# Optimization experiments

Measured on AMD Instinct MI355X. Metric: run time of the kernel, lower is better.

The kernel has to match this reference:

```python
import jax, jax.numpy as jnp
import numpy as np

N = 100000        # num nodes
E = 3_200_000     # num edges
NFEAT, NHID, NCLASS = 256, 128, 40
BN_EPS = 1e-5


def _gcn_norm(edge_index, edge_weight, num_nodes):
    """PyG gcn_norm with self-loops (fill value 1.0): returns (src, dst, norm)."""
    loop = jnp.arange(num_nodes)
    src = jnp.concatenate([edge_index[0], loop])
    dst = jnp.concatenate([edge_index[1], loop])
    ew = jnp.concatenate([edge_weight, jnp.ones((num_nodes,), edge_weight.dtype)])
    deg = jax.ops.segment_sum(ew, dst, num_segments=num_nodes)
    dinv = jnp.where(deg > 0, jax.lax.rsqrt(jnp.maximum(deg, 1e-30)), 0.0)
    norm = dinv[src] * ew * dinv[dst]  # [E+N]
    return src, dst, norm


def _gcn_layer(h, W, b, src, dst, norm, num_nodes):
    lin = h @ W                                   # [N, out]
    msg = lin[src] * norm[:, None]                # gather + scale  [E+N, out]
    agg = jax.ops.segment_sum(msg, dst, num_segments=num_nodes)
    return agg + b


def _bn(h, gamma, beta):
    # BatchNorm1d in training mode: biased batch statistics
    m = jnp.mean(h, axis=0)
    v = jnp.mean(jnp.square(h - m), axis=0)
    return (h - m) * jax.lax.rsqrt(v + BN_EPS) * gamma + beta


def setup_inputs() -> dict:
    key = jax.random.key(0)
    ks = jax.random.split(key, 12)
    s_in = 1.0 / np.sqrt(NFEAT)
    s_h = 1.0 / np.sqrt(NHID)
    return {
        "x": jax.random.normal(ks[0], (N, NFEAT), jnp.float32),
        "edge_index": jax.random.randint(ks[1], (2, E), 0, N, dtype=jnp.int32),
        "edge_weight": jax.random.uniform(ks[2], (E,), jnp.float32),
        "W1": jax.random.normal(ks[3], (NFEAT, NHID), jnp.float32) * s_in,
        "b1": jnp.zeros((NHID,), jnp.float32),
        "g1": jnp.ones((NHID,), jnp.float32),
        "beta1": jnp.zeros((NHID,), jnp.float32),
        "W2": jax.random.normal(ks[4], (NHID, NHID), jnp.float32) * s_h,
        "b2": jnp.zeros((NHID,), jnp.float32),
        "g2": jnp.ones((NHID,), jnp.float32),
        "beta2": jnp.zeros((NHID,), jnp.float32),
        "W3": jax.random.normal(ks[5], (NHID, NHID), jnp.float32) * s_h,
        "b3": jnp.zeros((NHID,), jnp.float32),
        "g3": jnp.ones((NHID,), jnp.float32),
        "beta3": jnp.zeros((NHID,), jnp.float32),
        "linW": jax.random.normal(ks[6], (3 * NHID, NCLASS), jnp.float32) / np.sqrt(3 * NHID),
        "linb": jnp.zeros((NCLASS,), jnp.float32),
    }


def reference(x, edge_index, edge_weight,
              W1, b1, g1, beta1,
              W2, b2, g2, beta2,
              W3, b3, g3, beta3,
              linW, linb):
    src, dst, norm = _gcn_norm(edge_index, edge_weight, N)
    x1 = _bn(jax.nn.relu(_gcn_layer(x, W1, b1, src, dst, norm, N)), g1, beta1)
    x2 = _bn(jax.nn.relu(_gcn_layer(x1, W2, b2, src, dst, norm, N)), g2, beta2)
    x3 = _bn(_gcn_layer(x2, W3, b3, src, dst, norm, N), g3, beta3)  # note: no relu on x3
    embed_x = jnp.concatenate([x1, x2, x3], axis=1)  # [N, 3*NHID]
    logits = embed_x @ linW + linb                   # [N, NCLASS]
    return logits, jax.nn.softmax(logits, axis=1), embed_x
```

## Files before the change

kernel.cpp:

```cpp
#include <hip/hip_runtime.h>
#include <hip/hip_bf16.h>
#include <hip/hip_fp16.h>
#include <math.h>

#define NN 100000
#define NE 3200000
#define NF 256
#define NH 128
#define NC 40
#define BN_EPS 1e-5f
#define NB 98

typedef __attribute__((ext_vector_type(8))) short bf16x8;
typedef __attribute__((ext_vector_type(4))) float f32x4;

__device__ __forceinline__ float2 bf2_unpack(unsigned int v) {
    return make_float2(__uint_as_float(v << 16), __uint_as_float(v & 0xffff0000u));
}
__device__ __forceinline__ unsigned int pack2bf(float lo, float hi) {
    unsigned int a = (unsigned int)__hip_bfloat16_raw(__float2bfloat16(lo)).x;
    unsigned int b = (unsigned int)__hip_bfloat16_raw(__float2bfloat16(hi)).x;
    return a | (b << 16);
}
__device__ __forceinline__ float4 affine4(float4 v, float4 sc, float4 sh) {
    v.x = fmaf(v.x, sc.x, sh.x);
    v.y = fmaf(v.y, sc.y, sh.y);
    v.z = fmaf(v.z, sc.z, sh.z);
    v.w = fmaf(v.w, sc.w, sh.w);
    return v;
}

__global__ __launch_bounds__(256) void k_init(unsigned long long* hist, float* sums) {
    int i = blockIdx.x * 256 + threadIdx.x;
    if (i < NN) hist[i] = 0ULL;
    if (i < 3 * 1024) sums[i] = 0.0f;
}

__global__ __launch_bounds__(256) void k_edge(const int* __restrict__ ei, const float* __restrict__ ew,
                                              unsigned long long* __restrict__ hist,
                                              unsigned int* __restrict__ pos) {
    int e = blockIdx.x * 256 + threadIdx.x;
    if (e >= NE) return;
    int d = __builtin_nontemporal_load(&ei[NE + e]);
    float w = __builtin_nontemporal_load(&ew[e]);
    unsigned long long pack = (1ULL << 44) | (unsigned long long)(w * 4294967296.0f);
    unsigned long long old = atomicAdd(&hist[d], pack);
    unsigned int h16 = (unsigned int)__half_as_ushort(__float2half(w));
    __builtin_nontemporal_store((unsigned int)(old >> 44) | (h16 << 16), &pos[e]);
}

__global__ __launch_bounds__(256) void k_scanA(const unsigned long long* __restrict__ hist,
                                               int* __restrict__ partial,
                                               float* __restrict__ dinv) {
    __shared__ int ws[4];
    int t = threadIdx.x;
    int i0 = blockIdx.x * 1024 + t * 4;
    int s = 0;
#pragma unroll
    for (int j = 0; j < 4; j++) {
        int i = i0 + j;
        if (i < NN) {
            unsigned long long h = hist[i];
            s += (int)(h >> 44);
            float wsum = (float)(h & 0xFFFFFFFFFFFULL) * 2.3283064365386963e-10f;
            dinv[i] = rsqrtf(1.0f + wsum);
        }
    }
#pragma unroll
    for (int off = 32; off >= 1; off >>= 1) s += __shfl_xor(s, off);
    if ((t & 63) == 0) ws[t >> 6] = s;
    __syncthreads();
    if (t == 0) partial[blockIdx.x] = ws[0] + ws[1] + ws[2] + ws[3];
}

__global__ void k_scanB(int* __restrict__ partial, int* __restrict__ rowptr) {
    __shared__ int buf[128];
    int t = threadIdx.x;
    buf[t] = (t < NB) ? partial[t] : 0;
    __syncthreads();
    if (t == 0) {
        int r = 0;
        for (int b = 0; b < NB; b++) { int v = buf[b]; buf[b] = r; r += v; }
        rowptr[NN] = r;
    }
    __syncthreads();
    if (t < NB) partial[t] = buf[t];
}

__global__ __launch_bounds__(256) void k_scanC(const unsigned long long* __restrict__ hist,
                                               const int* __restrict__ partial,
                                               int* __restrict__ rowptr) {
    __shared__ int wsum[4];
    int t = threadIdx.x;
    int lane = t & 63, wid = t >> 6;
    int i0 = blockIdx.x * 1024 + t * 4;
    int c[4];
#pragma unroll
    for (int j = 0; j < 4; j++) {
        int i = i0 + j;
        c[j] = (i < NN) ? (int)(hist[i] >> 44) : 0;
    }
    int v = c[0] + c[1] + c[2] + c[3];
    int x = v;
#pragma unroll
    for (int off = 1; off < 64; off <<= 1) {
        int y = __shfl_up(x, off);
        if (lane >= off) x += y;
    }
    if (lane == 63) wsum[wid] = x;
    __syncthreads();
    if (t == 0) {
        int r = 0;
#pragma unroll
        for (int w2 = 0; w2 < 4; w2++) { int s = wsum[w2]; wsum[w2] = r; r += s; }
    }
    __syncthreads();
    int start = partial[blockIdx.x] + wsum[wid] + x - v;
#pragma unroll
    for (int j = 0; j < 4; j++) {
        int i = i0 + j;
        if (i < NN) rowptr[i] = start;
        start += c[j];
    }
}

__global__ __launch_bounds__(256) void k_scatter(const int* __restrict__ ei,
                                                 const float* __restrict__ dinv,
                                                 const int* __restrict__ rowptr,
                                                 const unsigned int* __restrict__ pos,
                                                 unsigned int* __restrict__ cw) {
    int e = blockIdx.x * 256 + threadIdx.x;
    if (e >= NE) return;
    int s = __builtin_nontemporal_load(&ei[e]);
    int d = __builtin_nontemporal_load(&ei[NE + e]);
    unsigned int pw = __builtin_nontemporal_load(&pos[e]);
    float w = __half2float(__ushort_as_half((unsigned short)(pw >> 16)));
    float nv = dinv[s] * w * dinv[d];
    unsigned int h = (unsigned int)__half_as_ushort(__float2half(nv)) & 0x7fffu;
    unsigned int packed = (unsigned int)s | (h << 17);
    __builtin_nontemporal_store(packed, &cw[rowptr[d] + (int)(pw & 0xFFFFu)]);
}

template <int K, bool BN>
__device__ __forceinline__ void gemm_body(unsigned int (*Bt)[20], const float* H, float* Hw,
                                          const float* scp, const float* shp, int ldh,
                                          const float* W, __hip_bfloat16* out, int blk, int t) {
    int wid = t >> 6, l = t & 63;
    int l15 = l & 15, lhi = l >> 4;
    int rowbase = blk * 128 + wid * 32;
    bool ok0 = (rowbase + l15) < NN;
    bool ok1 = (rowbase + 16 + l15) < NN;
    int ar0 = rowbase + l15;      if (ar0 >= NN) ar0 = NN - 1;
    int ar1 = rowbase + 16 + l15; if (ar1 >= NN) ar1 = NN - 1;

    f32x4 acc[2][8];
#pragma unroll
    for (int rt = 0; rt < 2; rt++)
#pragma unroll
        for (int ct = 0; ct < 8; ct++) acc[rt][ct] = (f32x4){0.f, 0.f, 0.f, 0.f};

    for (int kb = 0; kb < K / 32; kb++) {
        __syncthreads();
        for (int i = t; i < 2048; i += 256) {
            int c = i & 127, k2l = i >> 7;
            int k = kb * 32 + 2 * k2l;
            Bt[c][k2l] = pack2bf(W[(size_t)k * NH + c], W[(size_t)(k + 1) * NH + c]);
        }
        __syncthreads();
        int kk = kb * 32 + lhi * 8;
        const float4* a0p = (const float4*)&H[(size_t)ar0 * ldh + kk];
        const float4* a1p = (const float4*)&H[(size_t)ar1 * ldh + kk];
        float4 x0 = a0p[0], x1 = a0p[1];
        float4 y0 = a1p[0], y1 = a1p[1];
        if constexpr (BN) {
            float4 sc0 = *(const float4*)&scp[kk];
            float4 sc1 = *(const float4*)&scp[kk + 4];
            float4 sh0 = *(const float4*)&shp[kk];
            float4 sh1 = *(const float4*)&shp[kk + 4];
            x0 = affine4(x0, sc0, sh0); x1 = affine4(x1, sc1, sh1);
            y0 = affine4(y0, sc0, sh0); y1 = affine4(y1, sc1, sh1);
            if (ok0) {
                *(float4*)&Hw[(size_t)ar0 * ldh + kk] = x0;
                *(float4*)&Hw[(size_t)ar0 * ldh + kk + 4] = x1;
            }
            if (ok1) {
                *(float4*)&Hw[(size_t)ar1 * ldh + kk] = y0;
                *(float4*)&Hw[(size_t)ar1 * ldh + kk + 4] = y1;
            }
        }
        union { unsigned int u[4]; bf16x8 v; } af0, af1;
        af0.u[0] = pack2bf(x0.x, x0.y); af0.u[1] = pack2bf(x0.z, x0.w);
        af0.u[2] = pack2bf(x1.x, x1.y); af0.u[3] = pack2bf(x1.z, x1.w);
        af1.u[0] = pack2bf(y0.x, y0.y); af1.u[1] = pack2bf(y0.z, y0.w);
        af1.u[2] = pack2bf(y1.x, y1.y); af1.u[3] = pack2bf(y1.z, y1.w);
#pragma unroll
        for (int ct = 0; ct < 8; ct++) {
            bf16x8 b = *(const bf16x8*)&Bt[ct * 16 + l15][lhi * 4];
            acc[0][ct] = __builtin_amdgcn_mfma_f32_16x16x32_bf16(af0.v, b, acc[0][ct], 0, 0, 0);
            acc[1][ct] = __builtin_amdgcn_mfma_f32_16x16x32_bf16(af1.v, b, acc[1][ct], 0, 0, 0);
        }
    }
#pragma unroll
    for (int rt = 0; rt < 2; rt++)
#pragma unroll
        for (int ct = 0; ct < 8; ct++)
#pragma unroll
            for (int reg = 0; reg < 4; reg++) {
                int row = rowbase + rt * 16 + lhi * 4 + reg;
                if (row < NN)
                    out[(size_t)row * NH + ct * 16 + l15] = __float2bfloat16(acc[rt][ct][reg]);
            }
}

__global__ __launch_bounds__(256) void k_gemm1(const float* __restrict__ H,
                                               const float* __restrict__ W,
                                               __hip_bfloat16* __restrict__ out) {
    __shared__ unsigned int Bt[128][20];
    gemm_body<NF, false>(Bt, H, nullptr, nullptr, nullptr, NF, W, out, (int)blockIdx.x, (int)threadIdx.x);
}

__global__ __launch_bounds__(256) void k_gemm_bn(const float* H, float* Hw,
                                                 const float* __restrict__ sums,
                                                 const float* __restrict__ g,
                                                 const float* __restrict__ beta,
                                                 const float* __restrict__ W,
                                                 __hip_bfloat16* __restrict__ out) {
    __shared__ unsigned int Bt[128][20];
    __shared__ __align__(16) float scL[128];
    __shared__ __align__(16) float shL[128];
    int t = threadIdx.x;
    if (t < 128) {
        float m = sums[t] * (1.0f / NN);
        float v = sums[NH + t] * (1.0f / NN) - m * m;
        float r = rsqrtf(v + BN_EPS);
        float sc = g[t] * r;
        scL[t] = sc;
        shL[t] = beta[t] - m * sc;
    }
    __syncthreads();
    gemm_body<NH, true>(Bt, H, Hw, scL, shL, 384, W, out, (int)blockIdx.x, (int)threadIdx.x);
}

__global__ __launch_bounds__(256) void k_agg(const unsigned int* __restrict__ linb,
                                             const float* __restrict__ dinv,
                                             const int* __restrict__ rowptr,
                                             const unsigned int* __restrict__ cw,
                                             const float* __restrict__ bias,
                                             float* __restrict__ outp, int do_relu) {
    int t = threadIdx.x;
    int node = blockIdx.x * 4 + (t >> 6);
    if (node >= NN) return;
    int ch = t & 63;
    int c = ch << 1;
    float di = dinv[node];
    float2 sv = bf2_unpack(linb[(size_t)node * 64 + ch]);
    float a0 = fmaf(sv.x, di * di, bias[c]);
    float a1 = fmaf(sv.y, di * di, bias[c + 1]);
    int beg = rowptr[node], end = rowptr[node + 1];
    int j = beg;
    for (; j + 16 <= end; j += 16) {
        unsigned int pk[16];
#pragma unroll
        for (int q = 0; q < 16; q++) pk[q] = cw[j + q];
        unsigned int v[16];
#pragma unroll
        for (int q = 0; q < 16; q++) v[q] = linb[(size_t)(pk[q] & 0x1FFFFu) * 64 + ch];
#pragma unroll
        for (int q = 0; q < 16; q++) {
            float w = __half2float(__ushort_as_half((unsigned short)(pk[q] >> 17)));
            float2 f = bf2_unpack(v[q]);
            a0 = fmaf(f.x, w, a0);
            a1 = fmaf(f.y, w, a1);
        }
    }
    for (; j + 4 <= end; j += 4) {
        unsigned int pk[4];
#pragma unroll
        for (int q = 0; q < 4; q++) pk[q] = cw[j + q];
        unsigned int v[4];
#pragma unroll
        for (int q = 0; q < 4; q++) v[q] = linb[(size_t)(pk[q] & 0x1FFFFu) * 64 + ch];
#pragma unroll
        for (int q = 0; q < 4; q++) {
            float w = __half2float(__ushort_as_half((unsigned short)(pk[q] >> 17)));
            float2 f = bf2_unpack(v[q]);
            a0 = fmaf(f.x, w, a0);
            a1 = fmaf(f.y, w, a1);
        }
    }
    for (; j < end; j++) {
        unsigned int pk = cw[j];
        unsigned int vv = linb[(size_t)(pk & 0x1FFFFu) * 64 + ch];
        float w = __half2float(__ushort_as_half((unsigned short)(pk >> 17)));
        float2 f = bf2_unpack(vv);
        a0 = fmaf(f.x, w, a0);
        a1 = fmaf(f.y, w, a1);
    }
    if (do_relu) { a0 = fmaxf(a0, 0.f); a1 = fmaxf(a1, 0.f); }
    *(float2*)&outp[(size_t)node * 384 + c] = make_float2(a0, a1);
}

__global__ __launch_bounds__(256) void k_stats(const float* __restrict__ pre, float* __restrict__ sums) {
    int t = threadIdx.x;
    int c = t & 127, h = t >> 7;
    float s = 0.f, s2 = 0.f;
    for (int r = blockIdx.x * 2 + h; r < NN; r += gridDim.x * 2) {
        float v = pre[(size_t)r * 384 + c];
        s += v;
        s2 = fmaf(v, v, s2);
    }
    __shared__ float ls[256], ls2[256];
    ls[t] = s; ls2[t] = s2;
    __syncthreads();
    if (t < 128) {
        atomicAdd(&sums[c], ls[t] + ls[t + 128]);
        atomicAdd(&sums[NH + c], ls2[t] + ls2[t + 128]);
    }
}

__global__ __launch_bounds__(256) void k_final(const float* __restrict__ embed, float* embedW,
                                               const float* __restrict__ sums3,
                                               const float* __restrict__ g3,
                                               const float* __restrict__ be3,
                                               const float* __restrict__ linW,
                                               const float* __restrict__ linb,
                                               float* __restrict__ logits, float* __restrict__ probs) {
    __shared__ unsigned int Wt[3 * 16 * 196];
    __shared__ __align__(16) float scL[128];
    __shared__ __align__(16) float shL[128];
    int t = threadIdx.x;
    if (t < 128) {
        float m = sums3[t] * (1.0f / NN);
        float v = sums3[NH + t] * (1.0f / NN) - m * m;
        float r = rsqrtf(v + BN_EPS);
        float sc = g3[t] * r;
        scL[t] = sc;
        shL[t] = be3[t] - m * sc;
    }
    for (int i = t; i < 3 * 16 * 192; i += 256) {
        int ct = i / (16 * 192);
        int rem = i - ct * (16 * 192);
        int c = rem / 192, k2 = rem - c * 192;
        int col = ct * 16 + c;
        float lo = (col < NC) ? linW[(size_t)(2 * k2) * NC + col] : 0.f;
        float hi = (col < NC) ? linW[(size_t)(2 * k2 + 1) * NC + col] : 0.f;
        Wt[(ct * 16 + c) * 196 + k2] = pack2bf(lo, hi);
    }
    __syncthreads();

    int wid = t >> 6, l = t & 63;
    int rowbase = blockIdx.x * 64 + wid * 16;
    int l15 = l & 15, lhi = l >> 4;

    bool okA = (rowbase + l15) < NN;
    int arow = rowbase + l15;
    if (arow > NN - 1) arow = NN - 1;
    const float4* ap = (const float4*)&embed[(size_t)arow * 384 + lhi * 8];

    f32x4 acc0 = {0.f, 0.f, 0.f, 0.f};
    f32x4 acc1 = {0.f, 0.f, 0.f, 0.f};
    f32x4 acc2 = {0.f, 0.f, 0.f, 0.f};

    for (int kb = 0; kb < 12; kb++) {
        float4 a0 = ap[kb * 8];
        float4 a1 = ap[kb * 8 + 1];
        if (kb >= 8) {
            int kk = kb * 32 + lhi * 8 - 256;
            float4 sc0 = *(const float4*)&scL[kk];
            float4 sc1 = *(const float4*)&scL[kk + 4];
            float4 sh0 = *(const float4*)&shL[kk];
            float4 sh1 = *(const float4*)&shL[kk + 4];
            a0 = affine4(a0, sc0, sh0);
            a1 = affine4(a1, sc1, sh1);
            if (okA) {
                *(float4*)&embedW[(size_t)arow * 384 + kb * 32 + lhi * 8] = a0;
                *(float4*)&embedW[(size_t)arow * 384 + kb * 32 + lhi * 8 + 4] = a1;
            }
        }
        union { unsigned int u[4]; bf16x8 v; } af;
        af.u[0] = pack2bf(a0.x, a0.y);
        af.u[1] = pack2bf(a0.z, a0.w);
        af.u[2] = pack2bf(a1.x, a1.y);
        af.u[3] = pack2bf(a1.z, a1.w);
        int wbase = kb * 16 + lhi * 4;
        bf16x8 b0 = *(const bf16x8*)&Wt[(0 * 16 + l15) * 196 + wbase];
        bf16x8 b1 = *(const bf16x8*)&Wt[(1 * 16 + l15) * 196 + wbase];
        bf16x8 b2 = *(const bf16x8*)&Wt[(2 * 16 + l15) * 196 + wbase];
        acc0 = __builtin_amdgcn_mfma_f32_16x16x32_bf16(af.v, b0, acc0, 0, 0, 0);
        acc1 = __builtin_amdgcn_mfma_f32_16x16x32_bf16(af.v, b1, acc1, 0, 0, 0);
        acc2 = __builtin_amdgcn_mfma_f32_16x16x32_bf16(af.v, b2, acc2, 0, 0, 0);
    }

    int col0 = 0 * 16 + l15, col1 = 1 * 16 + l15, col2 = 2 * 16 + l15;
    float lb0 = (col0 < NC) ? linb[col0] : 0.f;
    float lb1 = (col1 < NC) ? linb[col1] : 0.f;
    float lb2 = (col2 < NC) ? linb[col2] : 0.f;

#pragma unroll
    for (int reg = 0; reg < 4; reg++) {
        int row = rowbase + lhi * 4 + reg;
        float v0 = acc0[reg] + lb0;
        float v1 = acc1[reg] + lb1;
        float v2 = acc2[reg] + lb2;
        float m = fmaxf(v0, v1);
        if (col2 < NC) m = fmaxf(m, v2);
#pragma unroll
        for (int off = 1; off < 16; off <<= 1) m = fmaxf(m, __shfl_xor(m, off));
        float e0 = __expf(v0 - m);
        float e1 = __expf(v1 - m);
        float e2 = (col2 < NC) ? __expf(v2 - m) : 0.f;
        float s = e0 + e1 + e2;
#pragma unroll
        for (int off = 1; off < 16; off <<= 1) s += __shfl_xor(s, off);
        float inv = 1.0f / s;
        if (row < NN) {
            size_t base = (size_t)row * NC;
            logits[base + col0] = v0;
            probs[base + col0] = e0 * inv;
            logits[base + col1] = v1;
            probs[base + col1] = e1 * inv;
            if (col2 < NC) {
                logits[base + col2] = v2;
                probs[base + col2] = e2 * inv;
            }
        }
    }
}

extern "C" void kernel_launch(void* const* d_in, const int* in_sizes, int n_in,
                              void* d_out, int out_size, void* d_ws, size_t ws_size,
                              hipStream_t stream) {
    const float* x    = (const float*)d_in[0];
    const int*   ei   = (const int*)d_in[1];
    const float* ew   = (const float*)d_in[2];
    const float* W1   = (const float*)d_in[3];
    const float* b1   = (const float*)d_in[4];
    const float* g1   = (const float*)d_in[5];
    const float* be1  = (const float*)d_in[6];
    const float* W2   = (const float*)d_in[7];
    const float* b2   = (const float*)d_in[8];
    const float* g2   = (const float*)d_in[9];
    const float* be2  = (const float*)d_in[10];
    const float* W3   = (const float*)d_in[11];
    const float* b3   = (const float*)d_in[12];
    const float* g3   = (const float*)d_in[13];
    const float* be3  = (const float*)d_in[14];
    const float* linW = (const float*)d_in[15];
    const float* linb = (const float*)d_in[16];

    float* out    = (float*)d_out;
    float* logits = out;
    float* probs  = out + (size_t)NN * NC;
    float* embed  = out + (size_t)2 * NN * NC;

    char* ws = (char*)d_ws;
    size_t off = 0;
    auto alloc = [&](size_t bytes) -> char* {
        char* p = ws + off;
        off = (off + bytes + 255) & ~(size_t)255;
        return p;
    };
    float*              dinv    = (float*)alloc((size_t)NN * 4);
    unsigned long long* hist    = (unsigned long long*)alloc((size_t)NN * 8);
    int*                rowptr  = (int*)alloc((size_t)(NN + 1) * 4);
    int*                partial = (int*)alloc(128 * 4);
    unsigned int*       cw      = (unsigned int*)alloc((size_t)NE * 4);
    __hip_bfloat16*     lin     = (__hip_bfloat16*)alloc((size_t)NN * NH * 2);
    unsigned int*       pos     = (unsigned int*)alloc((size_t)NE * 4);
    float*              sums    = (float*)alloc(3 * 1024 * 4);
    (void)ws_size; (void)in_sizes; (void)n_in; (void)out_size;

    int gN = (NN + 255) / 256;
    int gE = (NE + 255) / 256;
    int gM = (NN + 127) / 128;
    int gA = (NN + 3) / 4;
    int gF = (NN + 63) / 64;

    k_init<<<gN, 256, 0, stream>>>(hist, sums);
    k_edge<<<gE, 256, 0, stream>>>(ei, ew, hist, pos);
    k_scanA<<<NB, 256, 0, stream>>>(hist, partial, dinv);
    k_scanB<<<1, 128, 0, stream>>>(partial, rowptr);
    k_scanC<<<NB, 256, 0, stream>>>(hist, partial, rowptr);
    k_scatter<<<gE, 256, 0, stream>>>(ei, dinv, rowptr, pos, cw);

    k_gemm1<<<gM, 256, 0, stream>>>(x, W1, lin);
    k_agg<<<gA, 256, 0, stream>>>((const unsigned int*)lin, dinv, rowptr, cw, b1, embed + 0, 1);
    k_stats<<<1024, 256, 0, stream>>>(embed + 0, sums + 0);
    k_gemm_bn<<<gM, 256, 0, stream>>>(embed + 0, embed + 0, sums + 0, g1, be1, W2, lin);
    k_agg<<<gA, 256, 0, stream>>>((const unsigned int*)lin, dinv, rowptr, cw, b2, embed + 128, 1);
    k_stats<<<1024, 256, 0, stream>>>(embed + 128, sums + 1024);
    k_gemm_bn<<<gM, 256, 0, stream>>>(embed + 128, embed + 128, sums + 1024, g2, be2, W3, lin);
    k_agg<<<gA, 256, 0, stream>>>((const unsigned int*)lin, dinv, rowptr, cw, b3, embed + 256, 0);
    k_stats<<<1024, 256, 0, stream>>>(embed + 256, sums + 2048);
    k_final<<<gF, 256, 0, stream>>>(embed, embed, sums + 2048, g3, be3, linW, linb, logits, probs);
}
```

Baseline: 947.9 us.

## Fuse batch-norm statistics into aggregation kernel with slotted atomic partial sums

Removes the separate k_stats pass. Each aggregation block now reduces its four nodes' per-channel sum and sum-of-squares in shared memory and adds them atomically into one of 8 slot buffers, which the BN consumers sum when they read them. This avoids re-reading the three 100000x128 embedding slices, at the cost of 25000 blocks issuing atomics spread over 8 slots. The bounds check is dropped because the node count divides evenly by 4.

```diff
diff --git a/kernel.cpp b/kernel.cpp
--- a/kernel.cpp
+++ b/kernel.cpp
@@ -10,6 +10,7 @@
 #define NC 40
 #define BN_EPS 1e-5f
 #define NB 98
+#define NSLOT 8
 
 typedef __attribute__((ext_vector_type(8))) short bf16x8;
 typedef __attribute__((ext_vector_type(4))) float f32x4;
@@ -30,10 +31,10 @@
     return v;
 }
 
-__global__ __launch_bounds__(256) void k_init(unsigned long long* hist, float* sums) {
+__global__ __launch_bounds__(256) void k_init(unsigned long long* hist, float* sums8) {
     int i = blockIdx.x * 256 + threadIdx.x;
     if (i < NN) hist[i] = 0ULL;
-    if (i < 3 * 1024) sums[i] = 0.0f;
+    if (i < 3 * NSLOT * 256) sums8[i] = 0.0f;
 }
 
 __global__ __launch_bounds__(256) void k_edge(const int* __restrict__ ei, const float* __restrict__ ew,
@@ -220,7 +221,7 @@
 }
 
 __global__ __launch_bounds__(256) void k_gemm_bn(const float* H, float* Hw,
-                                                 const float* __restrict__ sums,
+                                                 const float* __restrict__ sums8,
                                                  const float* __restrict__ g,
                                                  const float* __restrict__ beta,
                                                  const float* __restrict__ W,
@@ -230,8 +231,14 @@
     __shared__ __align__(16) float shL[128];
     int t = threadIdx.x;
     if (t < 128) {
-        float m = sums[t] * (1.0f / NN);
-        float v = sums[NH + t] * (1.0f / NN) - m * m;
+        float s = 0.f, s2 = 0.f;
+#pragma unroll
+        for (int c = 0; c < NSLOT; c++) {
+            s += sums8[c * 256 + t];
+            s2 += sums8[c * 256 + 128 + t];
+        }
+        float m = s * (1.0f / NN);
+        float v = s2 * (1.0f / NN) - m * m;
         float r = rsqrtf(v + BN_EPS);
         float sc = g[t] * r;
         scL[t] = sc;
@@ -246,10 +253,11 @@
                                              const int* __restrict__ rowptr,
                                              const unsigned int* __restrict__ cw,
                                              const float* __restrict__ bias,
-                                             float* __restrict__ outp, int do_relu) {
+                                             float* __restrict__ outp,
+                                             float* __restrict__ sums8, int do_relu) {
     int t = threadIdx.x;
-    int node = blockIdx.x * 4 + (t >> 6);
-    if (node >= NN) return;
+    int wid = t >> 6;
+    int node = blockIdx.x * 4 + wid;
     int ch = t & 63;
     int c = ch << 1;
     float di = dinv[node];
@@ -298,28 +306,30 @@
     }
     if (do_relu) { a0 = fmaxf(a0, 0.f); a1 = fmaxf(a1, 0.f); }
     *(float2*)&outp[(size_t)node * 384 + c] = make_float2(a0, a1);
-}
-
-__global__ __launch_bounds__(256) void k_stats(const float* __restrict__ pre, float* __restrict__ sums) {
-    int t = threadIdx.x;
-    int c = t & 127, h = t >> 7;
-    float s = 0.f, s2 = 0.f;
-    for (int r = blockIdx.x * 2 + h; r < NN; r += gridDim.x * 2) {
-        float v = pre[(size_t)r * 384 + c];
-        s += v;
-        s2 = fmaf(v, v, s2);
-    }
-    __shared__ float ls[256], ls2[256];
-    ls[t] = s; ls2[t] = s2;
-    __syncthreads();
-    if (t < 128) {
-        atomicAdd(&sums[c], ls[t] + ls[t + 128]);
-        atomicAdd(&sums[NH + c], ls2[t] + ls2[t + 128]);
+
+    __shared__ float red[4][64][4];
+    red[wid][ch][0] = a0;
+    red[wid][ch][1] = a1;
+    red[wid][ch][2] = a0 * a0;
+    red[wid][ch][3] = a1 * a1;
+    __syncthreads();
+    if (t < 64) {
+        float S0 = 0.f, S1 = 0.f, Q0 = 0.f, Q1 = 0.f;
+#pragma unroll
+        for (int w2 = 0; w2 < 4; w2++) {
+            S0 += red[w2][t][0]; S1 += red[w2][t][1];
+            Q0 += red[w2][t][2]; Q1 += red[w2][t][3];
+        }
+        float* slot = sums8 + (blockIdx.x & (NSLOT - 1)) * 256;
+        atomicAdd(&slot[2 * t], S0);
+        atomicAdd(&slot[2 * t + 1], S1);
+        atomicAdd(&slot[128 + 2 * t], Q0);
+        atomicAdd(&slot[128 + 2 * t + 1], Q1);
     }
 }
 
 __global__ __launch_bounds__(256) void k_final(const float* __restrict__ embed, float* embedW,
-                                               const float* __restrict__ sums3,
+                                               const float* __restrict__ sums8,
                                                const float* __restrict__ g3,
                                                const float* __restrict__ be3,
                                                const float* __restrict__ linW,
@@ -330,8 +340,14 @@
     __shared__ __align__(16) float shL[128];
     int t = threadIdx.x;
     if (t < 128) {
-        float m = sums3[t] * (1.0f / NN);
-        float v = sums3[NH + t] * (1.0f / NN) - m * m;
+        float s = 0.f, s2 = 0.f;
+#pragma unroll
+        for (int c = 0; c < NSLOT; c++) {
+            s += sums8[c * 256 + t];
+            s2 += sums8[c * 256 + 128 + t];
+        }
+        float m = s * (1.0f / NN);
+        float v = s2 * (1.0f / NN) - m * m;
         float r = rsqrtf(v + BN_EPS);
         float sc = g3[t] * r;
         scL[t] = sc;
@@ -467,16 +483,16 @@
     unsigned int*       cw      = (unsigned int*)alloc((size_t)NE * 4);
     __hip_bfloat16*     lin     = (__hip_bfloat16*)alloc((size_t)NN * NH * 2);
     unsigned int*       pos     = (unsigned int*)alloc((size_t)NE * 4);
-    float*              sums    = (float*)alloc(3 * 1024 * 4);
+    float*              sums8   = (float*)alloc(3 * NSLOT * 256 * 4);
     (void)ws_size; (void)in_sizes; (void)n_in; (void)out_size;
 
     int gN = (NN + 255) / 256;
     int gE = (NE + 255) / 256;
     int gM = (NN + 127) / 128;
-    int gA = (NN + 3) / 4;
+    int gA = NN / 4;
     int gF = (NN + 63) / 64;
 
-    k_init<<<gN, 256, 0, stream>>>(hist, sums);
+    k_init<<<gN, 256, 0, stream>>>(hist, sums8);
     k_edge<<<gE, 256, 0, stream>>>(ei, ew, hist, pos);
     k_scanA<<<NB, 256, 0, stream>>>(hist, partial, dinv);
     k_scanB<<<1, 128, 0, stream>>>(partial, rowptr);
@@ -484,13 +500,14 @@
     k_scatter<<<gE, 256, 0, stream>>>(ei, dinv, rowptr, pos, cw);
 
     k_gemm1<<<gM, 256, 0, stream>>>(x, W1, lin);
-    k_agg<<<gA, 256, 0, stream>>>((const unsigned int*)lin, dinv, rowptr, cw, b1, embed + 0, 1);
-    k_stats<<<1024, 256, 0, stream>>>(embed + 0, sums + 0);
-    k_gemm_bn<<<gM, 256, 0, stream>>>(embed + 0, embed + 0, sums + 0, g1, be1, W2, lin);
-    k_agg<<<gA, 256, 0, stream>>>((const unsigned int*)lin, dinv, rowptr, cw, b2, embed + 128, 1);
-    k_stats<<<1024, 256, 0, stream>>>(embed + 128, sums + 1024);
-    k_gemm_bn<<<gM, 256, 0, stream>>>(embed + 128, embed + 128, sums + 1024, g2, be2, W3, lin);
-    k_agg<<<gA, 256, 0, stream>>>((const unsigned int*)lin, dinv, rowptr, cw, b3, embed + 256, 0);
-    k_stats<<<1024, 256, 0, stream>>>(embed + 256, sums + 2048);
-    k_final<<<gF, 256, 0, stream>>>(embed, embed, sums + 2048, g3, be3, linW, linb, logits, probs);
-}
+    k_agg<<<gA, 256, 0, stream>>>((const unsigned int*)lin, dinv, rowptr, cw, b1, embed + 0,
+                                  sums8 + 0 * NSLOT * 256, 1);
+    k_gemm_bn<<<gM, 256, 0, stream>>>(embed + 0, embed + 0, sums8 + 0 * NSLOT * 256, g1, be1, W2, lin);
+    k_agg<<<gA, 256, 0, stream>>>((const unsigned int*)lin, dinv, rowptr, cw, b2, embed + 128,
+                                  sums8 + 1 * NSLOT * 256, 1);
+    k_gemm_bn<<<gM, 256, 0, stream>>>(embed + 128, embed + 128, sums8 + 1 * NSLOT * 256, g2, be2, W3, lin);
+    k_agg<<<gA, 256, 0, stream>>>((const unsigned int*)lin, dinv, rowptr, cw, b3, embed + 256,
+                                  sums8 + 2 * NSLOT * 256, 0);
+    k_final<<<gF, 256, 0, stream>>>(embed, embed, sums8 + 2 * NSLOT * 256, g3, be3, linW, linb,
+                                    logits, probs);
+}
```

Result: slower. 1.034 ms (+9.1%).
